# Performance work log

Measured on AMD Instinct MI355X. Metric: run time of the kernel, lower is better.

## Reference

```python
import jax, jax.numpy as jnp
import numpy as np

DN = ('NCHW', 'OIHW', 'NCHW')
B, C, H, W = 4, 64, 256, 256
MIP = 8          # max(8, C // 32)
RED = C // 16    # CBAM reduced channels
PS = 8           # FSAS patch size


def conv2d(x, w, padding=0, groups=1):
    return jax.lax.conv_general_dilated(
        x, w, (1, 1), [(padding, padding), (padding, padding)],
        dimension_numbers=DN, feature_group_count=groups)


def bn_eval(x, g, b, eps=1e-5):
    # BatchNorm with init running stats (mean=0, var=1), eval mode
    return x / jnp.sqrt(1.0 + eps) * g[None, :, None, None] + b[None, :, None, None]


def h_swish(x):
    return x * jnp.clip(x + 3.0, 0.0, 6.0) / 6.0


def setup_inputs() -> dict:
    key = jax.random.key(0)
    ks = jax.random.split(key, 12)
    s = 0.05
    d = {
        'x': jax.random.normal(ks[0], (B, C, H, W), jnp.float32),
        # CoordAttention
        'ca_conv1_w': jax.random.normal(ks[1], (MIP, C, 1, 1), jnp.float32) * s,
        'ca_conv1_b': jnp.zeros((MIP,), jnp.float32),
        'ca_bn_g': jnp.ones((MIP,), jnp.float32),
        'ca_bn_b': jnp.zeros((MIP,), jnp.float32),
        'ca_convh_w': jax.random.normal(ks[2], (C, MIP, 1, 1), jnp.float32) * s,
        'ca_convh_b': jnp.zeros((C,), jnp.float32),
        'ca_convw_w': jax.random.normal(ks[3], (C, MIP, 1, 1), jnp.float32) * s,
        'ca_convw_b': jnp.zeros((C,), jnp.float32),
        # FSAS (bias=False)
        'fsas_hidden_w': jax.random.normal(ks[4], (6 * C, C, 1, 1), jnp.float32) * s,
        'fsas_dw_w': jax.random.normal(ks[5], (6 * C, 1, 3, 3), jnp.float32) * s,
        'fsas_proj_w': jax.random.normal(ks[6], (C, 2 * C, 1, 1), jnp.float32) * s,
        'ln_w': jnp.ones((2 * C,), jnp.float32),
        'ln_b': jnp.zeros((2 * C,), jnp.float32),
        # Fusion
        'fus_conv1_w': jax.random.normal(ks[7], (2 * C, 2 * C, 3, 3), jnp.float32) * s,
        'fus_bn1_g': jnp.ones((2 * C,), jnp.float32),
        'fus_bn1_b': jnp.zeros((2 * C,), jnp.float32),
        'fus_conv2_w': jax.random.normal(ks[8], (C, 2 * C, 1, 1), jnp.float32) * s,
        'fus_bn2_g': jnp.ones((C,), jnp.float32),
        'fus_bn2_b': jnp.zeros((C,), jnp.float32),
        # CBAM
        'cbam_mlp1_w': jax.random.normal(ks[9], (RED, C, 1, 1), jnp.float32) * s,
        'cbam_mlp2_w': jax.random.normal(ks[10], (C, RED, 1, 1), jnp.float32) * s,
        'cbam_sa_w': jax.random.normal(ks[11], (1, 2, 7, 7), jnp.float32) * s,
        'residual_scale': jnp.float32(0.1),
    }
    return d


def _forward(x, ca_conv1_w, ca_conv1_b, ca_bn_g, ca_bn_b, ca_convh_w, ca_convh_b,
             ca_convw_w, ca_convw_b, fsas_hidden_w, fsas_dw_w, fsas_proj_w, ln_w, ln_b,
             fus_conv1_w, fus_bn1_g, fus_bn1_b, fus_conv2_w, fus_bn2_g, fus_bn2_b,
             cbam_mlp1_w, cbam_mlp2_w, cbam_sa_w, residual_scale):
    b, c, h, w = x.shape
    c2 = 2 * c

    # ---- CoordAttention branch ----
    xh = jnp.mean(x, axis=3, keepdims=True)                       # [B,C,H,1]
    xw = jnp.mean(x, axis=2, keepdims=True).transpose(0, 1, 3, 2)  # [B,C,W,1]
    y = jnp.concatenate([xh, xw], axis=2)                          # [B,C,H+W,1]
    y = conv2d(y, ca_conv1_w) + ca_conv1_b[None, :, None, None]
    y = h_swish(bn_eval(y, ca_bn_g, ca_bn_b))
    yh, yw = y[:, :, :h], y[:, :, h:]
    yw = yw.transpose(0, 1, 3, 2)
    a_h = jax.nn.sigmoid(conv2d(yh, ca_convh_w) + ca_convh_b[None, :, None, None])
    a_w = jax.nn.sigmoid(conv2d(yw, ca_convw_w) + ca_convw_b[None, :, None, None])
    ca_out = x * a_h * a_w

    # ---- FSAS branch ----
    hid = conv2d(x, fsas_hidden_w)                                 # [B,6C,H,W]
    hid = conv2d(hid, fsas_dw_w, padding=1, groups=6 * c)          # depthwise 3x3
    q, k, v = jnp.split(hid, 3, axis=1)                            # each [B,2C,H,W]

    def patch(t):  # [B,2C,H,W] -> [B,2C,H/8,W/8,8,8]
        return t.reshape(b, c2, h // PS, PS, w // PS, PS).transpose(0, 1, 2, 4, 3, 5)

    qf = jnp.fft.rfft2(patch(q))
    kf = jnp.fft.rfft2(patch(k))
    o = jnp.fft.irfft2(qf * kf, s=(PS, PS))
    o = o.transpose(0, 1, 2, 4, 3, 5).reshape(b, c2, h, w)

    # WithBias LayerNorm over channel dim (per pixel)
    mu = jnp.mean(o, axis=1, keepdims=True)
    var = jnp.var(o, axis=1, keepdims=True)
    on = (o - mu) / jnp.sqrt(var + 1e-5) * ln_w[None, :, None, None] + ln_b[None, :, None, None]
    fsas_out = conv2d(v * on, fsas_proj_w)                         # [B,C,H,W]

    # ---- Fusion ----
    f = conv2d(jnp.concatenate([ca_out, fsas_out], axis=1), fus_conv1_w, padding=1)
    f = jax.nn.gelu(bn_eval(f, fus_bn1_g, fus_bn1_b), approximate=False)
    f = bn_eval(conv2d(f, fus_conv2_w), fus_bn2_g, fus_bn2_b)

    z = x + residual_scale * f

    # ---- CBAM ----
    avg = jnp.mean(z, axis=(2, 3), keepdims=True)
    mx = jnp.max(z, axis=(2, 3), keepdims=True)

    def mlp(t):
        return conv2d(jax.nn.relu(conv2d(t, cbam_mlp1_w)), cbam_mlp2_w)

    z = z * jax.nn.sigmoid(mlp(avg) + mlp(mx))
    sa = jnp.concatenate([jnp.mean(z, axis=1, keepdims=True),
                          jnp.max(z, axis=1, keepdims=True)], axis=1)
    z = z * jax.nn.sigmoid(conv2d(sa, cbam_sa_w, padding=3))
    return jax.nn.gelu(z, approximate=False)


def reference(x, ca_conv1_w, ca_conv1_b, ca_bn_g, ca_bn_b, ca_convh_w, ca_convh_b,
              ca_convw_w, ca_convw_b, fsas_hidden_w, fsas_dw_w, fsas_proj_w, ln_w, ln_b,
              fus_conv1_w, fus_bn1_g, fus_bn1_b, fus_conv2_w, fus_bn2_g, fus_bn2_b,
              cbam_mlp1_w, cbam_mlp2_w, cbam_sa_w, residual_scale):
    return _forward(x, ca_conv1_w, ca_conv1_b, ca_bn_g, ca_bn_b, ca_convh_w, ca_convh_b,
                    ca_convw_w, ca_convw_b, fsas_hidden_w, fsas_dw_w, fsas_proj_w, ln_w, ln_b,
                    fus_conv1_w, fus_bn1_g, fus_bn1_b, fus_conv2_w, fus_bn2_g, fus_bn2_b,
                    cbam_mlp1_w, cbam_mlp2_w, cbam_sa_w, residual_scale)
```

## Files before the change

kernel.cpp:

```cpp
#include <hip/hip_runtime.h>
#include <math.h>

#define B_ 4
#define C_ 64
#define C2_ 128
#define C6_ 384
#define H_ 256
#define Wd_ 256
#define HW_ 65536
#define MIP_ 8
#define BNINV 0.9999950000374994f

typedef short bf16x8 __attribute__((ext_vector_type(8)));
typedef float f32x4 __attribute__((ext_vector_type(4)));
typedef unsigned short u16x8 __attribute__((ext_vector_type(8)));
typedef unsigned short u16x4 __attribute__((ext_vector_type(4)));
typedef unsigned int   u32x4 __attribute__((ext_vector_type(4)));

__device__ __forceinline__ float sigm(float x){ return 1.f/(1.f+expf(-x)); }
__device__ __forceinline__ float gelu_f(float x){ return 0.5f*x*(1.f+erff(x*0.7071067811865476f)); }
__device__ __forceinline__ unsigned short bfrnd(float f){
  unsigned u = __float_as_uint(f);
  unsigned r = u + 0x7FFFu + ((u>>16)&1u);
  return (unsigned short)(r>>16);
}
__device__ __forceinline__ float bf2f(unsigned short s){
  return __uint_as_float(((unsigned)s)<<16);
}

__global__ void __launch_bounds__(256) k_xstat(const float* __restrict__ x,
                                               float* __restrict__ xh, float* __restrict__ xw){
  int plane = blockIdx.x;
  int tid = threadIdx.x;
  const float* p = x + (size_t)plane*HW_;
  float cs = 0.f;
  for(int h=0;h<256;h++) cs += p[h*256+tid];
  xw[plane*256+tid] = cs*(1.f/256.f);
  float rs = 0.f;
  const f32x4* pr4 = (const f32x4*)(p + (size_t)tid*256);
  #pragma unroll 8
  for(int w=0;w<64;w++){ f32x4 v = pr4[w]; rs += v[0]+v[1]+v[2]+v[3]; }
  xh[plane*256+tid] = rs*(1.f/256.f);
}

__global__ void k_ca_t(const float* __restrict__ xh, const float* __restrict__ xw,
                       const float* __restrict__ w1, const float* __restrict__ b1,
                       const float* __restrict__ bng, const float* __restrict__ bnb,
                       float* __restrict__ t){
  int idx = blockIdx.x*256 + threadIdx.x;
  int p = idx & 511; int m = (idx>>9)&7; int b = idx>>12;
  float acc = b1[m];
  #pragma unroll 8
  for(int c=0;c<C_;c++){
    float yv = (p<256) ? xh[(b*C_+c)*256 + p] : xw[(b*C_+c)*256 + (p-256)];
    acc += w1[m*C_+c]*yv;
  }
  float v = acc*BNINV*bng[m] + bnb[m];
  t[idx] = v * fminf(fmaxf(v+3.f,0.f),6.f)*(1.f/6.f);
}

__global__ void k_ca_a(const float* __restrict__ t,
                       const float* __restrict__ wh, const float* __restrict__ bh,
                       const float* __restrict__ ww, const float* __restrict__ bw,
                       float* __restrict__ ah, float* __restrict__ aw){
  int idx = blockIdx.x*256 + threadIdx.x;
  int p = idx & 511; int co = (idx>>9)&63; int b = idx>>15;
  bool isH = (p<256);
  const float* wm = isH ? wh : ww;
  float acc = isH ? bh[co] : bw[co];
  #pragma unroll
  for(int m=0;m<MIP_;m++) acc += wm[co*MIP_+m]*t[(b*MIP_+m)*512+p];
  float s = sigm(acc);
  if(isH) ah[(b*C_+co)*256+p] = s; else aw[(b*C_+co)*256+(p-256)] = s;
}

__global__ void __launch_bounds__(256) k_xprep(const float* __restrict__ x, unsigned short* __restrict__ xb){
  __shared__ float sm[64][65];
  int tid = threadIdx.x;
  int img = blockIdx.x >> 10;
  int p0 = (blockIdx.x & 1023)*64;
  int lane = tid & 63, wq = tid >> 6;
  #pragma unroll
  for(int cc=0; cc<16; ++cc){
    int c = cc*4 + wq;
    sm[c][lane] = x[(size_t)(img*C_+c)*HW_ + p0 + lane];
  }
  __syncthreads();
  int pl = tid >> 2;
  int c0 = (tid & 3) * 16;
  u16x8 lo, hi;
  #pragma unroll
  for(int i=0;i<8;i++)  lo[i] = bfrnd(sm[c0+i][pl]);
  #pragma unroll
  for(int i=0;i<8;i++)  hi[i] = bfrnd(sm[c0+8+i][pl]);
  unsigned short* dst = xb + ((size_t)img*HW_ + p0 + pl)*64 + c0;
  *(u16x8*)(dst)     = lo;
  *(u16x8*)(dst + 8) = hi;
}

__global__ void k_wprep(const float* __restrict__ w, unsigned short* __restrict__ wbt){
  int t = blockIdx.x*256 + threadIdx.x;
  const float* src = w + (size_t)t*9;
  int oc = t >> 7, ic = t & 127;
  #pragma unroll
  for(int tap=0; tap<9; ++tap)
    wbt[(size_t)(tap*128+oc)*128 + ic] = bfrnd(src[tap]);
}

__global__ void k_wprep2(const float* __restrict__ pw, const float* __restrict__ w2,
                         const float* __restrict__ hw, unsigned short* __restrict__ pwb,
                         unsigned short* __restrict__ w2b, unsigned short* __restrict__ wb1){
  int t = blockIdx.x*256 + threadIdx.x;
  if(t < 8192){ pwb[t] = bfrnd(pw[t]); w2b[t] = bfrnd(w2[t]); }
  wb1[t] = bfrnd(hw[t]);
}

__global__ void __launch_bounds__(256) k_hid0_mfma(const unsigned short* __restrict__ xb,
                                                   const unsigned short* __restrict__ wb1,
                                                   unsigned short* __restrict__ hid0b){
  int tid = threadIdx.x;
  int lane = tid & 63, wid = tid >> 6;
  int l15 = lane & 15, lk = lane >> 4;
  int p0 = blockIdx.x*128 + wid*32;
  int oc0 = blockIdx.y*96;
  f32x4 acc[6][2];
  #pragma unroll
  for(int m=0;m<6;m++)
    #pragma unroll
    for(int n=0;n<2;n++) acc[m][n] = (f32x4)0.f;
  #pragma unroll
  for(int kk=0; kk<2; ++kk){
    bf16x8 bfr[2];
    #pragma unroll
    for(int n=0;n<2;n++)
      bfr[n] = *(const bf16x8*)(xb + (size_t)(p0 + n*16 + l15)*64 + kk*32 + lk*8);
    #pragma unroll
    for(int m=0;m<6;m++){
      bf16x8 af = *(const bf16x8*)(wb1 + (size_t)(oc0 + m*16 + l15)*64 + kk*32 + lk*8);
      #pragma unroll
      for(int n=0;n<2;n++)
        acc[m][n] = __builtin_amdgcn_mfma_f32_16x16x32_bf16(af, bfr[n], acc[m][n], 0,0,0);
    }
  }
  #pragma unroll
  for(int n=0;n<2;n++){
    int p = p0 + n*16 + l15;
    #pragma unroll
    for(int m=0;m<6;m++){
      u16x4 v;
      #pragma unroll
      for(int r=0;r<4;r++) v[r] = bfrnd(acc[m][n][r]);
      *(u16x4*)(hid0b + (size_t)p*384 + oc0 + m*16 + lk*4) = v;
    }
  }
}

__global__ void __launch_bounds__(256) k_dw_bf(const unsigned short* __restrict__ hid0b,
                                               const float* __restrict__ wd,
                                               unsigned short* __restrict__ hidb){
  int tid = threadIdx.x;
  int cg = tid & 15;
  int tg = tid >> 4;
  int p0 = blockIdx.x*64;
  int h  = p0 >> 8;
  int w0 = (p0 & 255) + tg*4;
  int chb = blockIdx.y*128 + cg*8;

  float wreg[72];
  {
    const f32x4* wsrc = (const f32x4*)(wd + (size_t)chb*9);
    #pragma unroll
    for(int i=0;i<18;i++){
      f32x4 v = wsrc[i];
      wreg[4*i+0]=v[0]; wreg[4*i+1]=v[1]; wreg[4*i+2]=v[2]; wreg[4*i+3]=v[3];
    }
  }
  float acc[4][8];
  #pragma unroll
  for(int px=0;px<4;px++)
    #pragma unroll
    for(int e=0;e<8;e++) acc[px][e] = 0.f;

  #pragma unroll
  for(int ky=0; ky<3; ++ky){
    int hh = h + ky - 1;
    if((unsigned)hh >= 256u) continue;
    float row[6][8];
    #pragma unroll
    for(int c6=0; c6<6; ++c6){
      int ww = w0 + c6 - 1;
      u16x8 v8 = {0,0,0,0,0,0,0,0};
      if((unsigned)ww < 256u)
        v8 = *(const u16x8*)(hid0b + (size_t)(hh*256+ww)*384 + chb);
      #pragma unroll
      for(int e=0;e<8;e++) row[c6][e] = bf2f(v8[e]);
    }
    #pragma unroll
    for(int kx=0; kx<3; ++kx){
      #pragma unroll
      for(int px=0; px<4; ++px){
        #pragma unroll
        for(int e=0;e<8;e++)
          acc[px][e] += row[px+kx][e] * wreg[e*9 + ky*3 + kx];
      }
    }
  }
  #pragma unroll
  for(int px=0; px<4; ++px){
    u16x8 o8;
    #pragma unroll
    for(int e=0;e<8;e++) o8[e] = bfrnd(acc[px][e]);
    *(u16x8*)(hidb + (size_t)(p0 + tg*4 + px)*384 + chb) = o8;
  }
}

__global__ void __launch_bounds__(256) k_circ_bf(const unsigned short* __restrict__ hidb,
                                                 unsigned short* __restrict__ ob){
  __shared__ __align__(16) unsigned short lq[2][64][128];
  __shared__ __align__(16) unsigned short lkk[2][64][128];
  int tid = threadIdx.x;
  #pragma unroll
  for(int it=0; it<8; ++it){
    int s = it*256 + tid;
    int which = s >> 10, rem = s & 1023;
    int pix = rem >> 4, cg = rem & 15;
    int gp = blockIdx.x*2 + which;
    int ph = gp >> 5, pw = gp & 31;
    size_t pg = (size_t)((ph*8 + (pix>>3))*256 + pw*8 + (pix&7));
    *(u16x8*)&lq[which][pix][cg*8]  = *(const u16x8*)(hidb + pg*384 + cg*8);
    *(u16x8*)&lkk[which][pix][cg*8] = *(const u16x8*)(hidb + pg*384 + 128 + cg*8);
  }
  __syncthreads();
  int which = tid >> 7, c = tid & 127;
  float kr[64];
  #pragma unroll
  for(int pix=0;pix<64;pix++) kr[pix] = bf2f(lkk[which][pix][c]);
  float outv[64];
  #pragma unroll
  for(int t2=0;t2<64;t2++) outv[t2] = 0.f;
  #pragma unroll
  for(int u=0;u<8;u++){
    #pragma unroll
    for(int v=0;v<8;v++){
      float qv = bf2f(lq[which][u*8+v][c]);
      #pragma unroll
      for(int i=0;i<8;i++){
        #pragma unroll
        for(int j=0;j<8;j++)
          outv[i*8+j] += qv * kr[((i-u)&7)*8 + ((j-v)&7)];
      }
    }
  }
  __syncthreads();
  #pragma unroll
  for(int t2=0;t2<64;t2++) lq[which][t2][c] = bfrnd(outv[t2]);
  __syncthreads();
  #pragma unroll
  for(int it=0; it<8; ++it){
    int s = it*256 + tid;
    int which2 = s >> 10, rem = s & 1023;
    int pix = rem >> 4, cg = rem & 15;
    int gp = blockIdx.x*2 + which2;
    int ph = gp >> 5, pw = gp & 31;
    size_t pg = (size_t)((ph*8 + (pix>>3))*256 + pw*8 + (pix&7));
    *(u16x8*)(ob + pg*128 + cg*8) = *(u16x8*)&lq[which2][pix][cg*8];
  }
}

__global__ void __launch_bounds__(256) k_proj_mfma(const unsigned short* __restrict__ ob,
                      const unsigned short* __restrict__ hidb,
                      const float* __restrict__ lnw, const float* __restrict__ lnb,
                      const unsigned short* __restrict__ pwb, unsigned short* __restrict__ catb){
  __shared__ unsigned int lds32[256*64];
  int tid = threadIdx.x;
  int lane = tid & 63, wid = tid >> 6;
  int p0 = blockIdx.x*256;
  {
    int p = p0 + tid;
    u16x8 o8[16];
    #pragma unroll
    for(int g=0; g<16; ++g) o8[g] = *(const u16x8*)(ob + (size_t)p*128 + g*8);
    float s=0.f, s2=0.f;
    #pragma unroll
    for(int g=0; g<16; ++g)
      #pragma unroll
      for(int e=0; e<8; ++e){ float v = bf2f(o8[g][e]); s += v; s2 += v*v; }
    float m = s*(1.f/C2_);
    float var = s2*(1.f/C2_) - m*m;
    float rs = rsqrtf(var + 1e-5f);
    #pragma unroll
    for(int cg=0; cg<16; ++cg){
      u16x8 v8 = *(const u16x8*)(hidb + (size_t)p*384 + 256 + cg*8);
      unsigned uu[4];
      #pragma unroll
      for(int ee=0; ee<4; ++ee){
        int c = cg*8 + ee*2;
        float on0 = (bf2f(o8[cg][2*ee])   - m)*rs*lnw[c]   + lnb[c];
        float on1 = (bf2f(o8[cg][2*ee+1]) - m)*rs*lnw[c+1] + lnb[c+1];
        float vn0 = bf2f(v8[2*ee])*on0;
        float vn1 = bf2f(v8[2*ee+1])*on1;
        uu[ee] = (unsigned)bfrnd(vn0) | ((unsigned)bfrnd(vn1)<<16);
      }
      int blk = cg ^ (tid & 15);
      u32x4 w4 = {uu[0],uu[1],uu[2],uu[3]};
      *(u32x4*)&lds32[tid*64 + blk*4] = w4;
    }
  }
  __syncthreads();
  int l15 = lane & 15, lk = lane >> 4;
  f32x4 acc[4][4];
  #pragma unroll
  for(int m=0;m<4;m++)
    #pragma unroll
    for(int n=0;n<4;n++) acc[m][n] = (f32x4)0.f;
  int plb = wid*64;
  #pragma unroll
  for(int kk=0; kk<4; ++kk){
    bf16x8 bfr[4];
    #pragma unroll
    for(int n=0;n<4;n++){
      int pl = plb + n*16 + l15;
      int blk = (kk*4 + lk) ^ l15;
      bfr[n] = *(bf16x8*)&lds32[pl*64 + blk*4];
    }
    #pragma unroll
    for(int m=0;m<4;m++){
      bf16x8 af = *(const bf16x8*)(pwb + (size_t)(m*16+l15)*128 + kk*32 + lk*8);
      #pragma unroll
      for(int n=0;n<4;n++)
        acc[m][n] = __builtin_amdgcn_mfma_f32_16x16x32_bf16(af, bfr[n], acc[m][n], 0,0,0);
    }
  }
  #pragma unroll
  for(int n=0;n<4;n++){
    int p = p0 + plb + n*16 + l15;
    #pragma unroll
    for(int m=0;m<4;m++){
      u16x4 v;
      #pragma unroll
      for(int r=0;r<4;r++) v[r] = bfrnd(acc[m][n][r]);
      *(u16x4*)(catb + (size_t)p*128 + 64 + m*16 + lk*4) = v;
    }
  }
}

__global__ void __launch_bounds__(256) k_caout_bf(const unsigned short* __restrict__ xb,
                        const float* __restrict__ ah, const float* __restrict__ aw,
                        unsigned short* __restrict__ catb, int b){
  __shared__ float ah_s[64];
  __shared__ float aw_s[64][65];
  int tid = threadIdx.x;
  int p0 = blockIdx.x*64;
  int h = p0 >> 8;
  int w0 = p0 & 255;
  if(tid < 64) ah_s[tid] = ah[(b*C_+tid)*256 + h];
  {
    int wl = tid & 63, cq = tid >> 6;
    #pragma unroll
    for(int cc=0; cc<16; ++cc){
      int c = cc*4 + cq;
      aw_s[c][wl] = aw[(b*C_+c)*256 + w0 + wl];
    }
  }
  __syncthreads();
  int pl = tid >> 2;
  int c0 = (tid & 3) * 16;
  u16x8 x0 = *(const u16x8*)(xb + (size_t)(p0+pl)*64 + c0);
  u16x8 x1 = *(const u16x8*)(xb + (size_t)(p0+pl)*64 + c0 + 8);
  u16x8 lo, hi;
  #pragma unroll
  for(int e=0;e<8;e++){
    lo[e] = bfrnd(bf2f(x0[e]) * ah_s[c0+e]   * aw_s[c0+e][pl]);
    hi[e] = bfrnd(bf2f(x1[e]) * ah_s[c0+8+e] * aw_s[c0+8+e][pl]);
  }
  unsigned short* dst = catb + (size_t)(p0+pl)*128 + c0;
  *(u16x8*)(dst)     = lo;
  *(u16x8*)(dst + 8) = hi;
}

__global__ void __launch_bounds__(256,3) k_fus1_mfma(const unsigned short* __restrict__ catb,
                                                     const unsigned short* __restrict__ wbt,
                                                     unsigned short* __restrict__ f1b){
  __shared__ __align__(16) unsigned short sA[3][130][32];
  int tid = threadIdx.x;
  int lane = tid & 63, wid = tid >> 6;
  int wm = wid & 1, wn = wid >> 1;
  int bid = blockIdx.x;
  int xcd = bid & 7, idx = bid >> 3;
  int h   = xcd*32 + (idx >> 2);
  int w0  = ((idx >> 1) & 1) * 128;
  int ocb = (idx & 1) * 64 + wn*32;
  int l15 = lane & 15, lk = lane >> 4;

  int srow[7], spxl[7], sicq[7];
  bool sok[7], sld[7];
  #pragma unroll
  for(int it=0; it<7; ++it){
    int s = it*256 + tid;
    sok[it] = (s < 1560);
    int row = s/520;
    int rem = s - row*520;
    int pxl = rem >> 2;
    int icq = rem & 3;
    srow[it]=row; spxl[it]=pxl; sicq[it]=icq;
    int r = h + row - 1;
    int c = w0 + pxl - 1;
    sld[it] = sok[it] && (unsigned)r < 256u && (unsigned)c < 256u;
  }

  u16x8 st[7];
  #pragma unroll
  for(int it=0; it<7; ++it){
    u16x8 v = {0,0,0,0,0,0,0,0};
    if(sld[it]){
      int r = h + srow[it] - 1, c = w0 + spxl[it] - 1;
      v = *(const u16x8*)(catb + (size_t)(r*256 + c)*128 + sicq[it]*8);
    }
    st[it] = v;
  }

  f32x4 acc[4][2];
  #pragma unroll
  for(int i=0;i<4;i++)
    #pragma unroll
    for(int j=0;j<2;j++) acc[i][j] = (f32x4)0.f;

  const unsigned short* wbase = wbt + (size_t)(ocb + l15)*128 + lk*8;

  for(int icc=0; icc<4; ++icc){
    int ic0 = icc*32;
    __syncthreads();
    #pragma unroll
    for(int it=0; it<7; ++it){
      if(sok[it]){
        int blk = sicq[it] ^ ((spxl[it]>>1)&3);
        *(u16x8*)&sA[srow[it]][spxl[it]][blk*8] = st[it];
      }
    }
    __syncthreads();
    if(icc < 3){
      int ic0n = (icc+1)*32;
      #pragma unroll
      for(int it=0; it<7; ++it){
        u16x8 v = {0,0,0,0,0,0,0,0};
        if(sld[it]){
          int r = h + srow[it] - 1, c = w0 + spxl[it] - 1;
          v = *(const u16x8*)(catb + (size_t)(r*256 + c)*128 + ic0n + sicq[it]*8);
        }
        st[it] = v;
      }
    }
    #pragma unroll
    for(int ky=0; ky<3; ++ky){
      bf16x8 wf[3][2];
      #pragma unroll
      for(int kx=0; kx<3; ++kx){
        const unsigned short* wt = wbase + (size_t)(ky*3+kx)*16384 + ic0;
        wf[kx][0] = *(const bf16x8*)(wt);
        wf[kx][1] = *(const bf16x8*)(wt + 2048);
      }
      #pragma unroll
      for(int kx=0; kx<3; ++kx){
        #pragma unroll
        for(int i=0;i<4;++i){
          int rr = wm*64 + i*16 + l15 + kx;
          int blk = lk ^ ((rr>>1)&3);
          bf16x8 a = *(const bf16x8*)&sA[ky][rr][blk*8];
          acc[i][0] = __builtin_amdgcn_mfma_f32_16x16x32_bf16(wf[kx][0], a, acc[i][0], 0,0,0);
          acc[i][1] = __builtin_amdgcn_mfma_f32_16x16x32_bf16(wf[kx][1], a, acc[i][1], 0,0,0);
        }
      }
    }
  }
  #pragma unroll
  for(int i=0;i<4;i++){
    int sp = h*256 + w0 + wm*64 + i*16 + l15;
    #pragma unroll
    for(int j=0;j<2;j++){
      u16x4 v;
      #pragma unroll
      for(int r2=0;r2<4;r2++) v[r2] = bfrnd(acc[i][j][r2]);
      *(u16x4*)(f1b + (size_t)sp*128 + ocb + j*16 + lk*4) = v;
    }
  }
}

__global__ void __launch_bounds__(256) k_fus2_mfma(const unsigned short* __restrict__ f1b,
                      const float* __restrict__ x, const unsigned short* __restrict__ w2b,
                      const float* __restrict__ bn1g, const float* __restrict__ bn1b,
                      const float* __restrict__ bn2g, const float* __restrict__ bn2b,
                      const float* __restrict__ rscale, unsigned short* __restrict__ zb,
                      float* __restrict__ psum2, float* __restrict__ pmax2, int b){
  __shared__ unsigned int lds32[128*64];
  __shared__ float smp[4][4][16], smm[4][4][16];
  int tid = threadIdx.x;
  int lane = tid & 63, wid = tid >> 6;
  int p0 = blockIdx.x*128;
  int ic0 = (tid & 15) * 8;
  #pragma unroll
  for(int pass=0; pass<8; ++pass){
    int pl = pass*16 + (tid>>4);
    bf16x8 vv = *(const bf16x8*)(f1b + (size_t)(p0+pl)*128 + ic0);
    unsigned uu[4];
    #pragma unroll
    for(int ee=0; ee<4; ++ee){
      float f0 = bf2f((unsigned short)vv[2*ee])  *BNINV*bn1g[ic0+2*ee]   + bn1b[ic0+2*ee];
      float f1 = bf2f((unsigned short)vv[2*ee+1])*BNINV*bn1g[ic0+2*ee+1] + bn1b[ic0+2*ee+1];
      uu[ee] = (unsigned)bfrnd(gelu_f(f0)) | ((unsigned)bfrnd(gelu_f(f1))<<16);
    }
    int blk = (ic0>>3) ^ (pl&15);
    u32x4 w4 = {uu[0],uu[1],uu[2],uu[3]};
    *(u32x4*)&lds32[pl*64 + blk*4] = w4;
  }
  __syncthreads();
  int l15 = lane & 15, lk = lane >> 4;
  f32x4 acc[4][2];
  #pragma unroll
  for(int m=0;m<4;m++)
    #pragma unroll
    for(int n=0;n<2;n++) acc[m][n] = (f32x4)0.f;
  int pl0 = wid*32 + l15;
  #pragma unroll
  for(int kk=0; kk<4; ++kk){
    bf16x8 bfr[2];
    #pragma unroll
    for(int n=0;n<2;n++){
      int pl = pl0 + n*16;
      int blk = (kk*4 + lk) ^ l15;
      bfr[n] = *(bf16x8*)&lds32[pl*64 + blk*4];
    }
    #pragma unroll
    for(int m=0;m<4;m++){
      bf16x8 af = *(const bf16x8*)(w2b + (size_t)(m*16+l15)*128 + kk*32 + lk*8);
      #pragma unroll
      for(int n=0;n<2;n++)
        acc[m][n] = __builtin_amdgcn_mfma_f32_16x16x32_bf16(af, bfr[n], acc[m][n], 0,0,0);
    }
  }
  float rs = rscale[0];
  float ps[4][4], pm[4][4];
  #pragma unroll
  for(int m=0;m<4;m++)
    #pragma unroll
    for(int r=0;r<4;r++){ ps[m][r]=0.f; pm[m][r]=-INFINITY; }
  #pragma unroll
  for(int n=0;n<2;n++){
    int p = p0 + pl0 + n*16;
    #pragma unroll
    for(int m=0;m<4;m++){
      #pragma unroll
      for(int r=0;r<4;r++){
        int oc = m*16 + lk*4 + r;
        float f = acc[m][n][r]*BNINV*bn2g[oc] + bn2b[oc];
        float zv = x[(size_t)(b*C_+oc)*HW_ + p] + rs*f;
        zb[(size_t)oc*HW_ + p] = bfrnd(zv);
        ps[m][r] += zv; pm[m][r] = fmaxf(pm[m][r], zv);
      }
    }
  }
  #pragma unroll
  for(int off=1; off<16; off<<=1){
    #pragma unroll
    for(int m=0;m<4;m++)
      #pragma unroll
      for(int r=0;r<4;r++){
        ps[m][r] += __shfl_xor(ps[m][r], off, 64);
        pm[m][r] = fmaxf(pm[m][r], __shfl_xor(pm[m][r], off, 64));
      }
  }
  if(l15 == 0){
    #pragma unroll
    for(int m=0;m<4;m++)
      #pragma unroll
      for(int r=0;r<4;r++){
        smp[wid][lk][m*4+r] = ps[m][r];
        smm[wid][lk][m*4+r] = pm[m][r];
      }
  }
  __syncthreads();
  if(tid < 64){
    int m = tid>>4, lkg = (tid>>2)&3, r = tid&3;
    float s = 0.f, mx = -INFINITY;
    #pragma unroll
    for(int w=0;w<4;w++){
      s += smp[w][lkg][m*4+r];
      mx = fmaxf(mx, smm[w][lkg][m*4+r]);
    }
    psum2[blockIdx.x*64 + tid] = s;
    pmax2[blockIdx.x*64 + tid] = mx;
  }
}

__global__ void k_cbamred2(const float* __restrict__ psum2, const float* __restrict__ pmax2,
                           float* __restrict__ avgb4, float* __restrict__ maxb4){
  int c = blockIdx.x & 63; int b = blockIdx.x >> 6;
  const float* ps = psum2 + (size_t)b*32768;
  const float* pmx = pmax2 + (size_t)b*32768;
  int tid = threadIdx.x;
  float s = ps[(size_t)tid*64 + c] + ps[(size_t)(tid+256)*64 + c];
  float m = fmaxf(pmx[(size_t)tid*64 + c], pmx[(size_t)(tid+256)*64 + c]);
  __shared__ float ss[256], sm[256];
  ss[tid]=s; sm[tid]=m; __syncthreads();
  for(int off=128; off>0; off>>=1){
    if(tid<off){ ss[tid]+=ss[tid+off]; sm[tid]=fmaxf(sm[tid],sm[tid+off]); }
    __syncthreads();
  }
  if(tid==0){ avgb4[b*64+c]=ss[0]*(1.f/HW_); maxb4[b*64+c]=sm[0]; }
}

__global__ void k_cbammlp(const float* __restrict__ avgb4, const float* __restrict__ maxb4,
                          const float* __restrict__ w1, const float* __restrict__ w2,
                          float* __restrict__ catt4){
  __shared__ float h1s[4][8];
  int tid = threadIdx.x;
  int b = tid >> 6, cl = tid & 63;
  if(cl < 8){
    const float* src = (cl<4)? avgb4 + b*64 : maxb4 + b*64;
    int r = cl & 3;
    float s = 0.f;
    for(int c=0;c<C_;c++) s += w1[r*C_+c]*src[c];
    h1s[b][cl] = fmaxf(s,0.f);
  }
  __syncthreads();
  float a = 0.f;
  #pragma unroll
  for(int r=0;r<4;r++) a += w2[cl*4+r]*(h1s[b][r]+h1s[b][r+4]);
  catt4[b*64+cl] = sigm(a);
}

__global__ void k_chatt(const unsigned short* __restrict__ z4, const float* __restrict__ catt4,
                        float* __restrict__ samean4, float* __restrict__ samax4){
  int gp = blockIdx.x*256 + threadIdx.x;
  int b = gp >> 16; int p = gp & 65535;
  const unsigned short* zb = z4 + (size_t)b*C_*HW_;
  const float* ct = catt4 + b*64;
  float s = 0.f, m = -INFINITY;
  #pragma unroll 8
  for(int c=0;c<C_;c++){
    float v = bf2f(zb[(size_t)c*HW_+p])*ct[c];
    s += v; m = fmaxf(m,v);
  }
  samean4[gp] = s*(1.f/C_);
  samax4[gp] = m;
}

__global__ void k_saconv(const float* __restrict__ samean4, const float* __restrict__ samax4,
                         const float* __restrict__ saw, float* __restrict__ att4){
  int gp = blockIdx.x*256 + threadIdx.x;
  int b = gp >> 16; int p = gp & 65535;
  int base = b << 16;
  int h = p>>8, w = p&255;
  float acc = 0.f;
  #pragma unroll
  for(int ky=0;ky<7;ky++){
    int hh = h+ky-3; if((unsigned)hh>=256u) continue;
    #pragma unroll
    for(int kx=0;kx<7;kx++){
      int ww2 = w+kx-3; if((unsigned)ww2>=256u) continue;
      int q = base + hh*256+ww2;
      acc += samean4[q]*saw[ky*7+kx] + samax4[q]*saw[49+ky*7+kx];
    }
  }
  att4[gp] = sigm(acc);
}

__global__ void k_final(const unsigned short* __restrict__ z4, const float* __restrict__ catt4,
                        const float* __restrict__ att4, float* __restrict__ out){
  int gp = blockIdx.x*256 + threadIdx.x;
  int b = gp >> 16; int p = gp & 65535;
  int c = blockIdx.y;
  float v = bf2f(z4[((size_t)(b*C_+c))*HW_ + p]) * catt4[b*64+c] * att4[gp];
  out[((size_t)(b*C_+c))*HW_ + p] = gelu_f(v);
}

extern "C" void kernel_launch(void* const* d_in, const int* in_sizes, int n_in,
                              void* d_out, int out_size, void* d_ws, size_t ws_size,
                              hipStream_t stream){
  const float* x            = (const float*)d_in[0];
  const float* ca_conv1_w   = (const float*)d_in[1];
  const float* ca_conv1_b   = (const float*)d_in[2];
  const float* ca_bn_g      = (const float*)d_in[3];
  const float* ca_bn_b      = (const float*)d_in[4];
  const float* ca_convh_w   = (const float*)d_in[5];
  const float* ca_convh_b   = (const float*)d_in[6];
  const float* ca_convw_w   = (const float*)d_in[7];
  const float* ca_convw_b   = (const float*)d_in[8];
  const float* fsas_hidden_w= (const float*)d_in[9];
  const float* fsas_dw_w    = (const float*)d_in[10];
  const float* fsas_proj_w  = (const float*)d_in[11];
  const float* ln_w         = (const float*)d_in[12];
  const float* ln_b         = (const float*)d_in[13];
  const float* fus_conv1_w  = (const float*)d_in[14];
  const float* fus_bn1_g    = (const float*)d_in[15];
  const float* fus_bn1_b    = (const float*)d_in[16];
  const float* fus_conv2_w  = (const float*)d_in[17];
  const float* fus_bn2_g    = (const float*)d_in[18];
  const float* fus_bn2_b    = (const float*)d_in[19];
  const float* cbam_mlp1_w  = (const float*)d_in[20];
  const float* cbam_mlp2_w  = (const float*)d_in[21];
  const float* cbam_sa_w    = (const float*)d_in[22];
  const float* rscale       = (const float*)d_in[23];
  float* out = (float*)d_out;
  float* ws  = (float*)d_ws;

  float* xh      = ws + 0;
  float* xw      = ws + 65536;
  float* t       = ws + 131072;
  float* ah      = ws + 147456;
  float* aw      = ws + 212992;
  float* catt4   = ws + 278528;
  float* avgb4   = ws + 278784;
  float* maxb4   = ws + 279040;
  float* psum2   = ws + 279296;
  float* pmax2   = ws + 410368;
  float* samean4 = ws + 541440;
  float* samax4  = ws + 803584;
  float* att4    = ws + 1065728;
  float* big     = ws + 1327872;
  unsigned short* catb  = (unsigned short*)(big);
  unsigned short* f1b   = (unsigned short*)(big + 4194304);
  unsigned short* z4    = (unsigned short*)(big + 8388608);
  unsigned short* xb    = (unsigned short*)(big + 16777216);
  unsigned short* hid0b = (unsigned short*)(big + 25165824);
  unsigned short* hidb  = (unsigned short*)(big + 37748736);
  unsigned short* obuf  = (unsigned short*)(big + 50331648);
  unsigned short* wbt   = (unsigned short*)(big + 54525952);
  unsigned short* wb1   = (unsigned short*)(big + 54599680);
  unsigned short* pwb   = (unsigned short*)(big + 54611968);
  unsigned short* w2b   = (unsigned short*)(big + 54616064);

  k_xstat<<<256,256,0,stream>>>(x, xh, xw);
  k_ca_t<<<64,256,0,stream>>>(xh, xw, ca_conv1_w, ca_conv1_b, ca_bn_g, ca_bn_b, t);
  k_ca_a<<<512,256,0,stream>>>(t, ca_convh_w, ca_convh_b, ca_convw_w, ca_convw_b, ah, aw);
  k_xprep<<<4096,256,0,stream>>>(x, xb);
  k_wprep<<<64,256,0,stream>>>(fus_conv1_w, wbt);
  k_wprep2<<<96,256,0,stream>>>(fsas_proj_w, fus_conv2_w, fsas_hidden_w, pwb, w2b, wb1);

  for(int b=0;b<4;b++){
    k_hid0_mfma<<<dim3(512,4),256,0,stream>>>(xb + (size_t)b*HW_*64, wb1, hid0b);
    k_dw_bf<<<dim3(1024,3),256,0,stream>>>(hid0b, fsas_dw_w, hidb);
    k_circ_bf<<<512,256,0,stream>>>(hidb, obuf);
    k_proj_mfma<<<256,256,0,stream>>>(obuf, hidb, ln_w, ln_b, pwb, catb);
    k_caout_bf<<<1024,256,0,stream>>>(xb + (size_t)b*HW_*64, ah, aw, catb, b);
    k_fus1_mfma<<<1024,256,0,stream>>>(catb, wbt, f1b);
    k_fus2_mfma<<<512,256,0,stream>>>(f1b, x, w2b, fus_bn1_g, fus_bn1_b, fus_bn2_g, fus_bn2_b,
                                      rscale, z4 + (size_t)b*C_*HW_,
                                      psum2 + (size_t)b*32768, pmax2 + (size_t)b*32768, b);
  }

  k_cbamred2<<<256,256,0,stream>>>(psum2, pmax2, avgb4, maxb4);
  k_cbammlp<<<1,256,0,stream>>>(avgb4, maxb4, cbam_mlp1_w, cbam_mlp2_w, catt4);
  k_chatt<<<1024,256,0,stream>>>(z4, catt4, samean4, samax4);
  k_saconv<<<1024,256,0,stream>>>(samean4, samax4, cbam_sa_w, att4);
  k_final<<<dim3(1024,64),256,0,stream>>>(z4, catt4, att4, out);
}
```

Before: 766.1 us.

## Fuse FSAS circular patch correlation with LayerNorm and projection MFMA kernel

Merges the per-patch circular correlation kernel with the LayerNorm, value-multiply and projection GEMM kernel. The correlation output stays in LDS instead of going through a global bf16 buffer, which is then re-read. The LDS rows are padded to 136 to reduce bank conflicts, and the per-pixel LN work is split across two threads with a shuffle reduction. The cost is a longer kernel with more LDS reuse and syncs, and projection work per block is smaller (128 pixels), which may hurt MFMA efficiency and occupancy.

```diff
diff --git a/kernel.cpp b/kernel.cpp
--- a/kernel.cpp
+++ b/kernel.cpp
@@ -214,10 +214,11 @@
   }
 }
 
-__global__ void __launch_bounds__(256) k_circ_bf(const unsigned short* __restrict__ hidb,
-                                                 unsigned short* __restrict__ ob){
-  __shared__ __align__(16) unsigned short lq[2][64][128];
-  __shared__ __align__(16) unsigned short lkk[2][64][128];
+__global__ void __launch_bounds__(256) k_circproj(const unsigned short* __restrict__ hidb,
+                      const float* __restrict__ lnw, const float* __restrict__ lnb,
+                      const unsigned short* __restrict__ pwb, unsigned short* __restrict__ catb){
+  __shared__ __align__(16) unsigned short lq[2][64][136];
+  __shared__ __align__(16) unsigned short lkk[2][64][136];
   int tid = threadIdx.x;
   #pragma unroll
   for(int it=0; it<8; ++it){
@@ -255,91 +256,87 @@
   #pragma unroll
   for(int t2=0;t2<64;t2++) lq[which][t2][c] = bfrnd(outv[t2]);
   __syncthreads();
-  #pragma unroll
-  for(int it=0; it<8; ++it){
-    int s = it*256 + tid;
-    int which2 = s >> 10, rem = s & 1023;
-    int pix = rem >> 4, cg = rem & 15;
-    int gp = blockIdx.x*2 + which2;
-    int ph = gp >> 5, pw = gp & 31;
-    size_t pg = (size_t)((ph*8 + (pix>>3))*256 + pw*8 + (pix&7));
-    *(u16x8*)(ob + pg*128 + cg*8) = *(u16x8*)&lq[which2][pix][cg*8];
-  }
-}
-
-__global__ void __launch_bounds__(256) k_proj_mfma(const unsigned short* __restrict__ ob,
-                      const unsigned short* __restrict__ hidb,
-                      const float* __restrict__ lnw, const float* __restrict__ lnb,
-                      const unsigned short* __restrict__ pwb, unsigned short* __restrict__ catb){
-  __shared__ unsigned int lds32[256*64];
-  int tid = threadIdx.x;
-  int lane = tid & 63, wid = tid >> 6;
-  int p0 = blockIdx.x*256;
   {
-    int p = p0 + tid;
-    u16x8 o8[16];
-    #pragma unroll
-    for(int g=0; g<16; ++g) o8[g] = *(const u16x8*)(ob + (size_t)p*128 + g*8);
+    unsigned int* vnb = (unsigned int*)&lkk[0][0][0];
+    int pix2 = tid >> 1, half = tid & 1;
+    int wp = pix2 >> 6, pp = pix2 & 63;
+    u16x8 o8[8];
+    #pragma unroll
+    for(int j=0;j<8;j++) o8[j] = *(const u16x8*)&lq[wp][pp][half*64 + j*8];
     float s=0.f, s2=0.f;
     #pragma unroll
-    for(int g=0; g<16; ++g)
-      #pragma unroll
-      for(int e=0; e<8; ++e){ float v = bf2f(o8[g][e]); s += v; s2 += v*v; }
+    for(int j=0;j<8;j++)
+      #pragma unroll
+      for(int e=0;e<8;e++){ float v = bf2f(o8[j][e]); s += v; s2 += v*v; }
+    s  += __shfl_xor(s, 1, 64);
+    s2 += __shfl_xor(s2, 1, 64);
     float m = s*(1.f/C2_);
     float var = s2*(1.f/C2_) - m*m;
     float rs = rsqrtf(var + 1e-5f);
-    #pragma unroll
-    for(int cg=0; cg<16; ++cg){
-      u16x8 v8 = *(const u16x8*)(hidb + (size_t)p*384 + 256 + cg*8);
+    int gp = blockIdx.x*2 + wp;
+    int ph = gp >> 5, pw = gp & 31;
+    size_t pg = (size_t)((ph*8 + (pp>>3))*256 + pw*8 + (pp&7));
+    #pragma unroll
+    for(int j=0;j<8;j++){
+      int cg = half*8 + j;
+      u16x8 v8 = *(const u16x8*)(hidb + pg*384 + 256 + cg*8);
       unsigned uu[4];
       #pragma unroll
       for(int ee=0; ee<4; ++ee){
-        int c = cg*8 + ee*2;
-        float on0 = (bf2f(o8[cg][2*ee])   - m)*rs*lnw[c]   + lnb[c];
-        float on1 = (bf2f(o8[cg][2*ee+1]) - m)*rs*lnw[c+1] + lnb[c+1];
+        int cidx = cg*8 + ee*2;
+        float on0 = (bf2f(o8[j][2*ee])   - m)*rs*lnw[cidx]   + lnb[cidx];
+        float on1 = (bf2f(o8[j][2*ee+1]) - m)*rs*lnw[cidx+1] + lnb[cidx+1];
         float vn0 = bf2f(v8[2*ee])*on0;
         float vn1 = bf2f(v8[2*ee+1])*on1;
         uu[ee] = (unsigned)bfrnd(vn0) | ((unsigned)bfrnd(vn1)<<16);
       }
-      int blk = cg ^ (tid & 15);
+      int blk = cg ^ (pix2 & 15);
       u32x4 w4 = {uu[0],uu[1],uu[2],uu[3]};
-      *(u32x4*)&lds32[tid*64 + blk*4] = w4;
-    }
-  }
-  __syncthreads();
-  int l15 = lane & 15, lk = lane >> 4;
-  f32x4 acc[4][4];
-  #pragma unroll
-  for(int m=0;m<4;m++)
-    #pragma unroll
-    for(int n=0;n<4;n++) acc[m][n] = (f32x4)0.f;
-  int plb = wid*64;
-  #pragma unroll
-  for(int kk=0; kk<4; ++kk){
-    bf16x8 bfr[4];
-    #pragma unroll
-    for(int n=0;n<4;n++){
-      int pl = plb + n*16 + l15;
-      int blk = (kk*4 + lk) ^ l15;
-      bfr[n] = *(bf16x8*)&lds32[pl*64 + blk*4];
-    }
-    #pragma unroll
-    for(int m=0;m<4;m++){
-      bf16x8 af = *(const bf16x8*)(pwb + (size_t)(m*16+l15)*128 + kk*32 + lk*8);
-      #pragma unroll
-      for(int n=0;n<4;n++)
-        acc[m][n] = __builtin_amdgcn_mfma_f32_16x16x32_bf16(af, bfr[n], acc[m][n], 0,0,0);
-    }
-  }
-  #pragma unroll
-  for(int n=0;n<4;n++){
-    int p = p0 + plb + n*16 + l15;
-    #pragma unroll
-    for(int m=0;m<4;m++){
-      u16x4 v;
-      #pragma unroll
-      for(int r=0;r<4;r++) v[r] = bfrnd(acc[m][n][r]);
-      *(u16x4*)(catb + (size_t)p*128 + 64 + m*16 + lk*4) = v;
+      *(u32x4*)&vnb[pix2*64 + blk*4] = w4;
+    }
+  }
+  __syncthreads();
+  {
+    const unsigned int* vnb = (const unsigned int*)&lkk[0][0][0];
+    int lane = tid & 63, wid = tid >> 6;
+    int l15 = lane & 15, lk = lane >> 4;
+    f32x4 acc[4][2];
+    #pragma unroll
+    for(int m=0;m<4;m++)
+      #pragma unroll
+      for(int n=0;n<2;n++) acc[m][n] = (f32x4)0.f;
+    int pl0 = wid*32 + l15;
+    #pragma unroll
+    for(int kk=0; kk<4; ++kk){
+      bf16x8 bfr[2];
+      #pragma unroll
+      for(int n=0;n<2;n++){
+        int pl = pl0 + n*16;
+        int blk = (kk*4 + lk) ^ l15;
+        bfr[n] = *(bf16x8*)&vnb[pl*64 + blk*4];
+      }
+      #pragma unroll
+      for(int m=0;m<4;m++){
+        bf16x8 af = *(const bf16x8*)(pwb + (size_t)(m*16+l15)*128 + kk*32 + lk*8);
+        #pragma unroll
+        for(int n=0;n<2;n++)
+          acc[m][n] = __builtin_amdgcn_mfma_f32_16x16x32_bf16(af, bfr[n], acc[m][n], 0,0,0);
+      }
+    }
+    #pragma unroll
+    for(int n=0;n<2;n++){
+      int pl = pl0 + n*16;
+      int ws2 = pl >> 6, ps2 = pl & 63;
+      int gp = blockIdx.x*2 + ws2;
+      int ph = gp >> 5, pw = gp & 31;
+      size_t pg = (size_t)((ph*8 + (ps2>>3))*256 + pw*8 + (ps2&7));
+      #pragma unroll
+      for(int m=0;m<4;m++){
+        u16x4 v;
+        #pragma unroll
+        for(int r=0;r<4;r++) v[r] = bfrnd(acc[m][n][r]);
+        *(u16x4*)(catb + pg*128 + 64 + m*16 + lk*4) = v;
+      }
     }
   }
 }
@@ -723,11 +720,10 @@
   unsigned short* xb    = (unsigned short*)(big + 16777216);
   unsigned short* hid0b = (unsigned short*)(big + 25165824);
   unsigned short* hidb  = (unsigned short*)(big + 37748736);
-  unsigned short* obuf  = (unsigned short*)(big + 50331648);
-  unsigned short* wbt   = (unsigned short*)(big + 54525952);
-  unsigned short* wb1   = (unsigned short*)(big + 54599680);
-  unsigned short* pwb   = (unsigned short*)(big + 54611968);
-  unsigned short* w2b   = (unsigned short*)(big + 54616064);
+  unsigned short* wbt   = (unsigned short*)(big + 50331648);
+  unsigned short* wb1   = (unsigned short*)(big + 50405376);
+  unsigned short* pwb   = (unsigned short*)(big + 50417664);
+  unsigned short* w2b   = (unsigned short*)(big + 50421760);
 
   k_xstat<<<256,256,0,stream>>>(x, xh, xw);
   k_ca_t<<<64,256,0,stream>>>(xh, xw, ca_conv1_w, ca_conv1_b, ca_bn_g, ca_bn_b, t);
@@ -739,8 +735,7 @@
   for(int b=0;b<4;b++){
     k_hid0_mfma<<<dim3(512,4),256,0,stream>>>(xb + (size_t)b*HW_*64, wb1, hid0b);
     k_dw_bf<<<dim3(1024,3),256,0,stream>>>(hid0b, fsas_dw_w, hidb);
-    k_circ_bf<<<512,256,0,stream>>>(hidb, obuf);
-    k_proj_mfma<<<256,256,0,stream>>>(obuf, hidb, ln_w, ln_b, pwb, catb);
+    k_circproj<<<512,256,0,stream>>>(hidb, ln_w, ln_b, pwb, catb);
     k_caout_bf<<<1024,256,0,stream>>>(xb + (size_t)b*HW_*64, ah, aw, catb, b);
     k_fus1_mfma<<<1024,256,0,stream>>>(catb, wbt, f1b);
     k_fus2_mfma<<<512,256,0,stream>>>(f1b, x, w2b, fus_bn1_g, fus_bn1_b, fus_bn2_g, fus_bn2_b,
```

New measurement: 778.2 us. About the same (+1.6%).
